# Kernel tuning notes

Hardware: AMD Instinct MI355X
Metric: run time of the kernel (lower is better)

Reference implementation:

```python
import jax, jax.numpy as jnp
import numpy as np

D_MODEL = 2048
N_HEADS = 16
N_KV_HEADS = 4
HEAD_DIM = D_MODEL // N_HEADS  # 128
N_REP = N_HEADS // N_KV_HEADS  # 4
ROPE_BASE = 10000.0


def _rope_tables(T, head_dim, dtype):
    inv_freq = 1.0 / (ROPE_BASE ** (jnp.arange(0, head_dim, 2, dtype=jnp.float32) / head_dim))
    t = jnp.arange(T, dtype=jnp.float32)
    freqs = jnp.outer(t, inv_freq)               # [T, hd/2]
    emb = jnp.concatenate([freqs, freqs], axis=-1)  # [T, hd]
    return jnp.cos(emb).astype(dtype), jnp.sin(emb).astype(dtype)


def _rotate_half(x):
    x1, x2 = jnp.split(x, 2, axis=-1)
    return jnp.concatenate([-x2, x1], axis=-1)


def _apply_rope(x, cos, sin):
    # x: [B, H, T, hd]; cos/sin: [T, hd]
    return x * cos[None, None] + _rotate_half(x) * sin[None, None]


def setup_inputs() -> dict:
    key = jax.random.key(0)
    ks = jax.random.split(key, 5)
    B, T = 2, 2048
    s_in = 1.0 / np.sqrt(D_MODEL)
    return {
        "x": jax.random.normal(ks[0], (B, T, D_MODEL), jnp.float32),
        "Wq": jax.random.normal(ks[1], (D_MODEL, D_MODEL), jnp.float32) * s_in,
        "Wk": jax.random.normal(ks[2], (D_MODEL, N_KV_HEADS * HEAD_DIM), jnp.float32) * s_in,
        "Wv": jax.random.normal(ks[3], (D_MODEL, N_KV_HEADS * HEAD_DIM), jnp.float32) * s_in,
        "Wo": jax.random.normal(ks[4], (D_MODEL, D_MODEL), jnp.float32) * s_in,
    }


def reference(x, Wq, Wk, Wv, Wo):
    B, T, C = x.shape
    scale = HEAD_DIM ** -0.5
    q = (x @ Wq).reshape(B, T, N_HEADS, HEAD_DIM).transpose(0, 2, 1, 3)     # [B,H,T,hd]
    k = (x @ Wk).reshape(B, T, N_KV_HEADS, HEAD_DIM).transpose(0, 2, 1, 3)  # [B,Hkv,T,hd]
    v = (x @ Wv).reshape(B, T, N_KV_HEADS, HEAD_DIM).transpose(0, 2, 1, 3)
    cos, sin = _rope_tables(T, HEAD_DIM, x.dtype)
    q = _apply_rope(q, cos, sin)
    k = _apply_rope(k, cos, sin)
    # GQA: group query heads; avoid materializing expanded K/V
    qg = q.reshape(B, N_KV_HEADS, N_REP, T, HEAD_DIM)
    scores = jnp.einsum('bgrtd,bgsd->bgrts', qg, k) * scale                 # [B,Hkv,rep,T,S]
    causal = jnp.tril(jnp.ones((T, T), dtype=bool))
    scores = jnp.where(causal[None, None, None], scores, jnp.finfo(scores.dtype).min)
    attn = jax.nn.softmax(scores, axis=-1)
    out = jnp.einsum('bgrts,bgsd->bgrtd', attn, v)                          # [B,Hkv,rep,T,hd]
    out = out.reshape(B, N_HEADS, T, HEAD_DIM).transpose(0, 2, 1, 3).reshape(B, T, C)
    return out @ Wo, k, v
```

## Files before the change

kernel.cpp:

```cpp
#include <hip/hip_runtime.h>
#include <hip/hip_bf16.h>
#include <type_traits>


typedef short  short8 __attribute__((ext_vector_type(8)));
typedef float  f32x4  __attribute__((ext_vector_type(4)));
typedef float  f32x16 __attribute__((ext_vector_type(16)));

#define AS1(p) ((__attribute__((address_space(1))) void*)(p))
#define AS3(p) ((__attribute__((address_space(3))) void*)(p))

static __device__ inline short bf_bits(float f) {
    __hip_bfloat16 h = __float2bfloat16(f);
    return *reinterpret_cast<short*>(&h);
}

__global__ __launch_bounds__(256) void convert_x_kernel(
    const float* __restrict__ x, __hip_bfloat16* __restrict__ xb)
{
    int i = (blockIdx.x * 256 + threadIdx.x) * 4;
    float4 v = *reinterpret_cast<const float4*>(x + i);
    ushort4 o;
    o.x = (unsigned short)bf_bits(v.x);
    o.y = (unsigned short)bf_bits(v.y);
    o.z = (unsigned short)bf_bits(v.z);
    o.w = (unsigned short)bf_bits(v.w);
    *reinterpret_cast<ushort4*>(reinterpret_cast<unsigned short*>(xb) + i) = o;
}

__global__ void transpose_convert_kernel(
    const float* __restrict__ W, __hip_bfloat16* __restrict__ WT, int K, int N)
{
    __shared__ float tile[32][33];
    int n0 = blockIdx.x * 32, k0 = blockIdx.y * 32;
    int tx = threadIdx.x, ty = threadIdx.y;
#pragma unroll
    for (int i = 0; i < 32; i += 8)
        tile[ty + i][tx] = W[(size_t)(k0 + ty + i) * N + n0 + tx];
    __syncthreads();
#pragma unroll
    for (int i = 0; i < 32; i += 8)
        WT[(size_t)(n0 + ty + i) * K + k0 + tx] = __float2bfloat16(tile[tx][ty + i]);
}

static __device__ inline void xcd_decode(int bid, int M, int N, int& m0, int& n0)
{
    const int xcd = bid & 7;
    const int idx = bid >> 3;
    const int mpx = (M >> 7) >> 3;
    const int rem = idx % (mpx * 4);
    const int mb = xcd * mpx + rem % mpx;
    const int nb = (idx / (mpx * 4)) * 4 + rem / mpx;
    m0 = mb << 7;
    n0 = nb << 7;
}

#define WAITV4 asm volatile("s_waitcnt vmcnt(4)" ::: "memory")
#define WAITV0 asm volatile("s_waitcnt vmcnt(0)" ::: "memory")

template <typename CT>
__global__ __launch_bounds__(256) void gemm_bt_kernel(
    const __hip_bfloat16* __restrict__ A,
    const __hip_bfloat16* __restrict__ BT,
    CT* __restrict__ C, int M, int N, int K)
{
    const int tid  = threadIdx.x;
    const int w    = tid >> 6;
    const int lane = tid & 63;
    const int l31  = lane & 31;
    const int hi   = lane >> 5;
    int m0, n0;
    xcd_decode(blockIdx.x, M, N, m0, n0);
    const int wm = (w >> 1) << 6;
    const int wn = (w & 1) << 6;

    __shared__ __hip_bfloat16 As[2][128 * 64];
    __shared__ __hip_bfloat16 Bs[2][128 * 64];

    f32x16 acc[2][2] = {};

#define GSTAGE(buf, k0_)                                                            \
    {                                                                               \
        _Pragma("unroll")                                                           \
        for (int i = 0; i < 4; ++i) {                                               \
            int c = tid + i * 256;                                                  \
            int row = c >> 3;                                                       \
            int soct = (c & 7) ^ (row & 7);                                         \
            const __hip_bfloat16* ga = A  + (size_t)(m0 + row) * K + (k0_) + soct * 8; \
            const __hip_bfloat16* gb = BT + (size_t)(n0 + row) * K + (k0_) + soct * 8; \
            __builtin_amdgcn_global_load_lds(AS1(ga), AS3(&As[buf][c * 8]), 16, 0, 0); \
            __builtin_amdgcn_global_load_lds(AS1(gb), AS3(&Bs[buf][c * 8]), 16, 0, 0); \
        }                                                                           \
    }

    GSTAGE(0, 0);
    __syncthreads();
    int cur = 0;
    const int nk = K >> 6;

    for (int t = 0; t < nk; ++t) {
        if (t + 1 < nk) GSTAGE(cur ^ 1, (t + 1) << 6);

#pragma unroll
        for (int ks = 0; ks < 4; ++ks) {
            const int oct = ((ks * 2 + hi) ^ (l31 & 7)) << 3;
            short8 a[2], b[2];
#pragma unroll
            for (int mi = 0; mi < 2; ++mi)
                a[mi] = *reinterpret_cast<const short8*>(
                    reinterpret_cast<const short*>(&As[cur][0]) + (wm + mi * 32 + l31) * 64 + oct);
#pragma unroll
            for (int ni = 0; ni < 2; ++ni)
                b[ni] = *reinterpret_cast<const short8*>(
                    reinterpret_cast<const short*>(&Bs[cur][0]) + (wn + ni * 32 + l31) * 64 + oct);
#pragma unroll
            for (int mi = 0; mi < 2; ++mi)
#pragma unroll
                for (int ni = 0; ni < 2; ++ni)
                    acc[mi][ni] = __builtin_amdgcn_mfma_f32_32x32x16_bf16(
                        a[mi], b[ni], acc[mi][ni], 0, 0, 0);
        }
        __syncthreads();
        cur ^= 1;
    }
#undef GSTAGE

#pragma unroll
    for (int mi = 0; mi < 2; ++mi)
#pragma unroll
        for (int ni = 0; ni < 2; ++ni)
#pragma unroll
            for (int reg = 0; reg < 16; ++reg) {
                int row = m0 + wm + mi * 32 + (reg & 3) + 8 * (reg >> 2) + 4 * hi;
                int col = n0 + wn + ni * 32 + l31;
                float v = acc[mi][ni][reg];
                if constexpr (std::is_same<CT, float>::value)
                    C[(size_t)row * N + col] = v;
                else
                    C[(size_t)row * N + col] = __float2bfloat16(v);
            }
}

__global__ __launch_bounds__(256) void gemm_qkv_fused(
    const __hip_bfloat16* __restrict__ A,
    const __hip_bfloat16* __restrict__ BT,
    __hip_bfloat16* __restrict__ qkv,
    float* __restrict__ outk,
    float* __restrict__ outv,
    __hip_bfloat16* __restrict__ VT)
{
    const int tid  = threadIdx.x;
    const int w    = tid >> 6;
    const int lane = tid & 63;
    const int l31  = lane & 31;
    const int hi   = lane >> 5;
    int m0, n0;
    xcd_decode(blockIdx.x, 4096, 3072, m0, n0);
    const int wm = w << 5;
    const int K = 2048;

    __shared__ __hip_bfloat16 As[3][128 * 32];
    __shared__ __hip_bfloat16 Bs[3][128 * 32];

    f32x16 acc[4] = {};

#define GSTAGE(buf, k0_)                                                             \
    {                                                                                \
        _Pragma("unroll")                                                            \
        for (int i = 0; i < 2; ++i) {                                                \
            int c = tid + i * 256;                                                   \
            int row = c >> 2;                                                        \
            int soct = (c & 3) ^ ((row >> 1) & 3);                                   \
            const __hip_bfloat16* ga = A  + (size_t)(m0 + row) * K + (k0_) + soct * 8; \
            const __hip_bfloat16* gb = BT + (size_t)(n0 + row) * K + (k0_) + soct * 8; \
            __builtin_amdgcn_global_load_lds(AS1(ga), AS3(&As[buf][c * 8]), 16, 0, 0); \
            __builtin_amdgcn_global_load_lds(AS1(gb), AS3(&Bs[buf][c * 8]), 16, 0, 0); \
        }                                                                            \
    }

    const int nk = 64;
    GSTAGE(0, 0);
    GSTAGE(1, 32);
    int cur = 0, stg = 2;

    for (int t = 0; t < nk; ++t) {
        if (t == nk - 1) { WAITV0; } else { WAITV4; }
        __builtin_amdgcn_s_barrier();
        __builtin_amdgcn_sched_barrier(0);
        if (t + 2 < nk) GSTAGE(stg, (t + 2) << 5);

#pragma unroll
        for (int ks = 0; ks < 2; ++ks) {
            int arow = wm + l31;
            short8 a = *reinterpret_cast<const short8*>(
                reinterpret_cast<const short*>(&As[cur][0])
                + arow * 32 + (((ks * 2 + hi) ^ ((arow >> 1) & 3)) << 3));
#pragma unroll
            for (int ni = 0; ni < 4; ++ni) {
                int brow = ni * 32 + l31;
                short8 b = *reinterpret_cast<const short8*>(
                    reinterpret_cast<const short*>(&Bs[cur][0])
                    + brow * 32 + (((ks * 2 + hi) ^ ((brow >> 1) & 3)) << 3));
                acc[ni] = __builtin_amdgcn_mfma_f32_32x32x16_bf16(a, b, acc[ni], 0, 0, 0);
            }
        }
        cur = (cur == 2) ? 0 : cur + 1;
        stg = (stg == 2) ? 0 : stg + 1;
    }
#undef GSTAGE

    const int hc = n0 >> 7;
    if (hc < 20) {
        float invf[2];
#pragma unroll
        for (int ni = 0; ni < 2; ++ni)
            invf[ni] = exp2f((float)(ni * 32 + l31) * -0.20762050593046f);
#pragma unroll
        for (int reg = 0; reg < 16; ++reg) {
            int row = m0 + wm + (reg & 3) + 8 * (reg >> 2) + 4 * hi;
            int b = row >> 11, t = row & 2047;
#pragma unroll
            for (int ni = 0; ni < 2; ++ni) {
                int d = ni * 32 + l31;
                float ang = (float)t * invf[ni];
                float s = __sinf(ang), c = __cosf(ang);
                float x1 = acc[ni][reg], x2 = acc[ni + 2][reg];
                float o1 = x1 * c - x2 * s;
                float o2 = x2 * c + x1 * s;
                __hip_bfloat16* q = qkv + (size_t)row * 3072 + hc * 128 + d;
                q[0]  = __float2bfloat16(o1);
                q[64] = __float2bfloat16(o2);
                if (hc >= 16) {
                    int kh = hc - 16;
                    float* ok = outk + (size_t)((b * 4 + kh) * 2048 + t) * 128 + d;
                    ok[0]  = o1;
                    ok[64] = o2;
                }
            }
        }
    } else {
        const int kh = hc - 20;
#pragma unroll
        for (int reg = 0; reg < 16; ++reg) {
            int row = m0 + wm + (reg & 3) + 8 * (reg >> 2) + 4 * hi;
            int b = row >> 11, t = row & 2047;
#pragma unroll
            for (int ni = 0; ni < 4; ++ni) {
                int d = ni * 32 + l31;
                float v = acc[ni][reg];
                outv[(size_t)((b * 4 + kh) * 2048 + t) * 128 + d] = v;
                VT[(size_t)((b * 4 + kh) * 128 + d) * 2048 + t] = __float2bfloat16(v);
            }
        }
    }
}

__global__ __launch_bounds__(256, 2) void attn_kernel(
    const __hip_bfloat16* __restrict__ qkv,
    const __hip_bfloat16* __restrict__ VT,
    __hip_bfloat16* __restrict__ outO)
{
    const int bh = blockIdx.x;
    const int b = bh >> 4, h = bh & 15;
    const int kh = h >> 2;
    const int yb = blockIdx.y;
    const int qblk = (yb < 8) ? (15 - yb) : (yb - 8);
    const int tid = threadIdx.x;
    const int w = tid >> 6;
    const int lane = tid & 63;
    const int lo16 = lane & 15, grp = lane >> 4;
    const int qrow0 = qblk * 128 + w * 32;

    __shared__ short Ks[2][64 * 128];
    __shared__ short Vs[2][128 * 64];
    __shared__ short Ps[4][32 * 64];

    const short* qkvs = reinterpret_cast<const short*>(qkv);
    const size_t kbase = (size_t)b * 2048 * 3072 + 2048 + kh * 128;
    const short* vtb = reinterpret_cast<const short*>(VT) + (size_t)(b * 4 + kh) * 128 * 2048;
    short* pw = &Ps[w][0];

    short8 qf[2][4];
#pragma unroll
    for (int mi = 0; mi < 2; ++mi) {
        const short* qp = qkvs + (size_t)(b * 2048 + qrow0 + mi * 16 + lo16) * 3072
                        + h * 128 + grp * 8;
#pragma unroll
        for (int ss = 0; ss < 4; ++ss)
            qf[mi][ss] = *reinterpret_cast<const short8*>(qp + ss * 32);
    }

    f32x4 o[2][8] = {};
    f32x4 lac[2] = {};

    short8 ones;
#pragma unroll
    for (int jj = 0; jj < 8; ++jj) ones[jj] = (short)0x3F80;

    const float scl2 = 0.12752749545902973f;
    const int ntiles = qblk * 2 + 2;

#define STAGE(buf, kb_)                                                              \
    {                                                                                \
        _Pragma("unroll")                                                            \
        for (int i = 0; i < 4; ++i) {                                                \
            int c = tid + i * 256;                                                   \
            int row = c >> 4, c16 = (c & 15) ^ (row & 7);                            \
            const short* src = qkvs + kbase + (size_t)((kb_) + row) * 3072 + c16 * 8;\
            __builtin_amdgcn_global_load_lds(AS1(src),                               \
                AS3(&Ks[buf][(w * 64 + i * 256) * 8]), 16, 0, 0);                    \
        }                                                                            \
        _Pragma("unroll")                                                            \
        for (int i = 0; i < 4; ++i) {                                                \
            int c = tid + i * 256;                                                   \
            int d = c >> 3, c8 = (c & 7) ^ (d & 7);                                  \
            const short* src = vtb + (size_t)d * 2048 + (kb_) + c8 * 8;              \
            __builtin_amdgcn_global_load_lds(AS1(src),                               \
                AS3(&Vs[buf][(w * 64 + i * 256) * 8]), 16, 0, 0);                    \
        }                                                                            \
    }

    STAGE(0, 0);
    __syncthreads();
    int cur = 0;

    for (int t = 0; t < ntiles; ++t) {
        const int kb = t * 64;
        if (t + 1 < ntiles) STAGE(cur ^ 1, kb + 64);

        f32x4 sg[2][4];
        __builtin_amdgcn_s_setprio(1);
#pragma unroll
        for (int kg = 0; kg < 4; ++kg) {
            f32x4 a0 = {}, a1 = {};
#pragma unroll
            for (int ss = 0; ss < 4; ++ss) {
                short8 kf = *reinterpret_cast<const short8*>(
                    &Ks[cur][(kg * 16 + lo16) * 128 + (((ss * 4 + grp) ^ (lo16 & 7)) << 3)]);
                a0 = __builtin_amdgcn_mfma_f32_16x16x32_bf16(qf[0][ss], kf, a0, 0, 0, 0);
                a1 = __builtin_amdgcn_mfma_f32_16x16x32_bf16(qf[1][ss], kf, a1, 0, 0, 0);
            }
            sg[0][kg] = a0; sg[1][kg] = a1;
        }
        __builtin_amdgcn_s_setprio(0);

        if (kb + 63 > qrow0) {
#pragma unroll
            for (int mi = 0; mi < 2; ++mi)
#pragma unroll
                for (int kg = 0; kg < 4; ++kg) {
                    const int key = kb + kg * 16 + lo16;
#pragma unroll
                    for (int r = 0; r < 4; ++r) {
                        float v = sg[mi][kg][r] * scl2;
                        sg[mi][kg][r] = (key <= qrow0 + mi * 16 + grp * 4 + r) ? v : -1e30f;
                    }
                }
        } else {
#pragma unroll
            for (int mi = 0; mi < 2; ++mi)
#pragma unroll
                for (int kg = 0; kg < 4; ++kg)
#pragma unroll
                    for (int r = 0; r < 4; ++r) sg[mi][kg][r] *= scl2;
        }

#pragma unroll
        for (int mi = 0; mi < 2; ++mi)
#pragma unroll
            for (int kg = 0; kg < 4; ++kg)
#pragma unroll
                for (int r = 0; r < 4; ++r) {
                    float p = __builtin_amdgcn_exp2f(sg[mi][kg][r]);
                    int row = mi * 16 + grp * 4 + r;
                    int idx = row * 64 + (((kg * 2 + (lo16 >> 3)) ^ (row & 7)) << 3) + (lo16 & 7);
                    pw[idx] = bf_bits(p);
                }

        __builtin_amdgcn_s_setprio(1);
#pragma unroll
        for (int ks = 0; ks < 2; ++ks) {
            short8 pf0 = *reinterpret_cast<const short8*>(
                &pw[(0 * 16 + lo16) * 64 + (((ks * 4 + grp) ^ (lo16 & 7)) << 3)]);
            short8 pf1 = *reinterpret_cast<const short8*>(
                &pw[(1 * 16 + lo16) * 64 + (((ks * 4 + grp) ^ (lo16 & 7)) << 3)]);
            lac[0] = __builtin_amdgcn_mfma_f32_16x16x32_bf16(pf0, ones, lac[0], 0, 0, 0);
            lac[1] = __builtin_amdgcn_mfma_f32_16x16x32_bf16(pf1, ones, lac[1], 0, 0, 0);
#pragma unroll
            for (int jj = 0; jj < 8; ++jj) {
                short8 vf = *reinterpret_cast<const short8*>(
                    &Vs[cur][(jj * 16 + lo16) * 64 + (((ks * 4 + grp) ^ (lo16 & 7)) << 3)]);
                o[0][jj] = __builtin_amdgcn_mfma_f32_16x16x32_bf16(pf0, vf, o[0][jj], 0, 0, 0);
                o[1][jj] = __builtin_amdgcn_mfma_f32_16x16x32_bf16(pf1, vf, o[1][jj], 0, 0, 0);
            }
        }
        __builtin_amdgcn_s_setprio(0);

        __syncthreads();
        cur ^= 1;
    }
#undef STAGE

#pragma unroll
    for (int mi = 0; mi < 2; ++mi)
#pragma unroll
        for (int r = 0; r < 4; ++r) {
            float inv = 1.0f / lac[mi][r];
#pragma unroll
            for (int jj = 0; jj < 8; ++jj) {
                outO[(size_t)(b * 2048 + qrow0 + mi * 16 + grp * 4 + r) * 2048
                     + h * 128 + jj * 16 + lo16] = __float2bfloat16(o[mi][jj][r] * inv);
            }
        }
}

extern "C" void kernel_launch(void* const* d_in, const int* in_sizes, int n_in,
                              void* d_out, int out_size, void* d_ws, size_t ws_size,
                              hipStream_t stream)
{
    (void)in_sizes; (void)n_in; (void)out_size; (void)ws_size;
    const float* x  = (const float*)d_in[0];
    const float* Wq = (const float*)d_in[1];
    const float* Wk = (const float*)d_in[2];
    const float* Wv = (const float*)d_in[3];
    const float* Wo = (const float*)d_in[4];

    float* out0 = (float*)d_out;
    float* outk = out0 + 8388608;
    float* outv = out0 + 10485760;

    __hip_bfloat16* wsb    = (__hip_bfloat16*)d_ws;
    __hip_bfloat16* xb     = wsb;
    __hip_bfloat16* WqkvT  = xb + 8388608;
    __hip_bfloat16* WoT    = WqkvT + 6291456;
    __hip_bfloat16* qkv    = WoT + 4194304;
    __hip_bfloat16* VT     = qkv + 12582912;
    __hip_bfloat16* attn_o = xb;

    convert_x_kernel<<<8192, 256, 0, stream>>>(x, xb);
    transpose_convert_kernel<<<dim3(64, 64), dim3(32, 8), 0, stream>>>(Wq, WqkvT, 2048, 2048);
    transpose_convert_kernel<<<dim3(16, 64), dim3(32, 8), 0, stream>>>(Wk, WqkvT + (size_t)2048 * 2048, 2048, 512);
    transpose_convert_kernel<<<dim3(16, 64), dim3(32, 8), 0, stream>>>(Wv, WqkvT + (size_t)2560 * 2048, 2048, 512);
    transpose_convert_kernel<<<dim3(64, 64), dim3(32, 8), 0, stream>>>(Wo, WoT, 2048, 2048);

    gemm_qkv_fused<<<768, 256, 0, stream>>>(xb, WqkvT, qkv, outk, outv, VT);

    attn_kernel<<<dim3(32, 16), 256, 0, stream>>>(qkv, VT, attn_o);

    gemm_bt_kernel<float><<<512, 256, 0, stream>>>(attn_o, WoT, out0, 4096, 2048, 2048);
}
```

Baseline: 194.7 us.

## Use 2x2 wave tiling in QKV GEMM and merge weight transposes into one launch

The QKV GEMM's four waves now each own a 64x64 sub-tile (2x2 MFMA blocks) instead of 32x128, which lowers LDS fragment reads per MFMA. To keep RoPE pairs (d, d+64) inside one wave, the Wq/Wk transpose permutes 32-row blocks within each head. RoPE output is written back in that permuted column order, which the attention kernel is assumed to accept. The four weight transpose launches are also merged into a single grid, cutting launch overhead.

Measured after the change: 190.8 us. -2.0%, faster.

```diff
diff --git a/kernel.cpp b/kernel.cpp
--- a/kernel.cpp
+++ b/kernel.cpp
@@ -28,19 +28,42 @@
     *reinterpret_cast<ushort4*>(reinterpret_cast<unsigned short*>(xb) + i) = o;
 }
 
-__global__ void transpose_convert_kernel(
-    const float* __restrict__ W, __hip_bfloat16* __restrict__ WT, int K, int N)
+__global__ void transpose_all_kernel(
+    const float* __restrict__ Wq, const float* __restrict__ Wk,
+    const float* __restrict__ Wv, const float* __restrict__ Wo,
+    __hip_bfloat16* __restrict__ WqkvT, __hip_bfloat16* __restrict__ WoT)
 {
     __shared__ float tile[32][33];
-    int n0 = blockIdx.x * 32, k0 = blockIdx.y * 32;
-    int tx = threadIdx.x, ty = threadIdx.y;
+    const int nb = blockIdx.x;
+    const int k0 = blockIdx.y * 32;
+    const int tx = threadIdx.x, ty = threadIdx.y;
+    const float* W; int srcN, sn0, drow; __hip_bfloat16* dst;
+    if (nb < 64) {
+        int blk = nb & 3;
+        int blk2 = ((blk & 1) << 1) | (blk >> 1);
+        W = Wq; srcN = 2048; sn0 = nb * 32;
+        dst = WqkvT; drow = ((nb >> 2) * 4 + blk2) * 32;
+    } else if (nb < 80) {
+        int i = nb - 64, blk = i & 3;
+        int blk2 = ((blk & 1) << 1) | (blk >> 1);
+        W = Wk; srcN = 512; sn0 = i * 32;
+        dst = WqkvT; drow = 2048 + ((i >> 2) * 4 + blk2) * 32;
+    } else if (nb < 96) {
+        int i = nb - 80;
+        W = Wv; srcN = 512; sn0 = i * 32;
+        dst = WqkvT; drow = 2560 + i * 32;
+    } else {
+        int i = nb - 96;
+        W = Wo; srcN = 2048; sn0 = i * 32;
+        dst = WoT; drow = i * 32;
+    }
 #pragma unroll
     for (int i = 0; i < 32; i += 8)
-        tile[ty + i][tx] = W[(size_t)(k0 + ty + i) * N + n0 + tx];
+        tile[ty + i][tx] = W[(size_t)(k0 + ty + i) * srcN + sn0 + tx];
     __syncthreads();
 #pragma unroll
     for (int i = 0; i < 32; i += 8)
-        WT[(size_t)(n0 + ty + i) * K + k0 + tx] = __float2bfloat16(tile[tx][ty + i]);
+        dst[(size_t)(drow + ty + i) * 2048 + k0 + tx] = __float2bfloat16(tile[tx][ty + i]);
 }
 
 static __device__ inline void xcd_decode(int bid, int M, int N, int& m0, int& n0)
@@ -156,13 +179,14 @@
     const int hi   = lane >> 5;
     int m0, n0;
     xcd_decode(blockIdx.x, 4096, 3072, m0, n0);
-    const int wm = w << 5;
+    const int wm = (w >> 1) << 6;
+    const int wn = (w & 1) << 6;
     const int K = 2048;
 
     __shared__ __hip_bfloat16 As[3][128 * 32];
     __shared__ __hip_bfloat16 Bs[3][128 * 32];
 
-    f32x16 acc[4] = {};
+    f32x16 acc[2][2] = {};
 
 #define GSTAGE(buf, k0_)                                                             \
     {                                                                                \
@@ -191,18 +215,27 @@
 
 #pragma unroll
         for (int ks = 0; ks < 2; ++ks) {
-            int arow = wm + l31;
-            short8 a = *reinterpret_cast<const short8*>(
-                reinterpret_cast<const short*>(&As[cur][0])
-                + arow * 32 + (((ks * 2 + hi) ^ ((arow >> 1) & 3)) << 3));
-#pragma unroll
-            for (int ni = 0; ni < 4; ++ni) {
-                int brow = ni * 32 + l31;
-                short8 b = *reinterpret_cast<const short8*>(
+            short8 a[2], b[2];
+#pragma unroll
+            for (int mi = 0; mi < 2; ++mi) {
+                int row = wm + mi * 32 + l31;
+                a[mi] = *reinterpret_cast<const short8*>(
+                    reinterpret_cast<const short*>(&As[cur][0])
+                    + row * 32 + (((ks * 2 + hi) ^ ((row >> 1) & 3)) << 3));
+            }
+#pragma unroll
+            for (int ni = 0; ni < 2; ++ni) {
+                int row = wn + ni * 32 + l31;
+                b[ni] = *reinterpret_cast<const short8*>(
                     reinterpret_cast<const short*>(&Bs[cur][0])
-                    + brow * 32 + (((ks * 2 + hi) ^ ((brow >> 1) & 3)) << 3));
-                acc[ni] = __builtin_amdgcn_mfma_f32_32x32x16_bf16(a, b, acc[ni], 0, 0, 0);
-            }
+                    + row * 32 + (((ks * 2 + hi) ^ ((row >> 1) & 3)) << 3));
+            }
+#pragma unroll
+            for (int mi = 0; mi < 2; ++mi)
+#pragma unroll
+                for (int ni = 0; ni < 2; ++ni)
+                    acc[mi][ni] = __builtin_amdgcn_mfma_f32_32x32x16_bf16(
+                        a[mi], b[ni], acc[mi][ni], 0, 0, 0);
         }
         cur = (cur == 2) ? 0 : cur + 1;
         stg = (stg == 2) ? 0 : stg + 1;
@@ -211,47 +244,46 @@
 
     const int hc = n0 >> 7;
     if (hc < 20) {
-        float invf[2];
-#pragma unroll
-        for (int ni = 0; ni < 2; ++ni)
-            invf[ni] = exp2f((float)(ni * 32 + l31) * -0.20762050593046f);
-#pragma unroll
-        for (int reg = 0; reg < 16; ++reg) {
-            int row = m0 + wm + (reg & 3) + 8 * (reg >> 2) + 4 * hi;
-            int b = row >> 11, t = row & 2047;
-#pragma unroll
-            for (int ni = 0; ni < 2; ++ni) {
-                int d = ni * 32 + l31;
-                float ang = (float)t * invf[ni];
+        const int c0 = wn + l31;
+        const int d_lo = (wn ? 32 : 0) + l31;
+        const float invf = exp2f((float)d_lo * -0.20762050593046f);
+        const int kh = hc - 16;
+#pragma unroll
+        for (int mi = 0; mi < 2; ++mi)
+#pragma unroll
+            for (int reg = 0; reg < 16; ++reg) {
+                int row = m0 + wm + mi * 32 + (reg & 3) + 8 * (reg >> 2) + 4 * hi;
+                int b = row >> 11, t = row & 2047;
+                float ang = (float)t * invf;
                 float s = __sinf(ang), c = __cosf(ang);
-                float x1 = acc[ni][reg], x2 = acc[ni + 2][reg];
+                float x1 = acc[mi][0][reg], x2 = acc[mi][1][reg];
                 float o1 = x1 * c - x2 * s;
                 float o2 = x2 * c + x1 * s;
-                __hip_bfloat16* q = qkv + (size_t)row * 3072 + hc * 128 + d;
+                __hip_bfloat16* q = qkv + (size_t)row * 3072 + hc * 128 + c0;
                 q[0]  = __float2bfloat16(o1);
-                q[64] = __float2bfloat16(o2);
+                q[32] = __float2bfloat16(o2);
                 if (hc >= 16) {
-                    int kh = hc - 16;
-                    float* ok = outk + (size_t)((b * 4 + kh) * 2048 + t) * 128 + d;
+                    float* ok = outk + (size_t)((b * 4 + kh) * 2048 + t) * 128 + d_lo;
                     ok[0]  = o1;
                     ok[64] = o2;
                 }
             }
-        }
     } else {
         const int kh = hc - 20;
 #pragma unroll
-        for (int reg = 0; reg < 16; ++reg) {
-            int row = m0 + wm + (reg & 3) + 8 * (reg >> 2) + 4 * hi;
-            int b = row >> 11, t = row & 2047;
-#pragma unroll
-            for (int ni = 0; ni < 4; ++ni) {
-                int d = ni * 32 + l31;
-                float v = acc[ni][reg];
-                outv[(size_t)((b * 4 + kh) * 2048 + t) * 128 + d] = v;
-                VT[(size_t)((b * 4 + kh) * 128 + d) * 2048 + t] = __float2bfloat16(v);
-            }
-        }
+        for (int mi = 0; mi < 2; ++mi)
+#pragma unroll
+            for (int reg = 0; reg < 16; ++reg) {
+                int row = m0 + wm + mi * 32 + (reg & 3) + 8 * (reg >> 2) + 4 * hi;
+                int b = row >> 11, t = row & 2047;
+#pragma unroll
+                for (int ni = 0; ni < 2; ++ni) {
+                    int d = wn + ni * 32 + l31;
+                    float v = acc[mi][ni][reg];
+                    outv[(size_t)((b * 4 + kh) * 2048 + t) * 128 + d] = v;
+                    VT[(size_t)((b * 4 + kh) * 128 + d) * 2048 + t] = __float2bfloat16(v);
+                }
+            }
     }
 }
 
@@ -438,10 +470,8 @@
     __hip_bfloat16* attn_o = xb;
 
     convert_x_kernel<<<8192, 256, 0, stream>>>(x, xb);
-    transpose_convert_kernel<<<dim3(64, 64), dim3(32, 8), 0, stream>>>(Wq, WqkvT, 2048, 2048);
-    transpose_convert_kernel<<<dim3(16, 64), dim3(32, 8), 0, stream>>>(Wk, WqkvT + (size_t)2048 * 2048, 2048, 512);
-    transpose_convert_kernel<<<dim3(16, 64), dim3(32, 8), 0, stream>>>(Wv, WqkvT + (size_t)2560 * 2048, 2048, 512);
-    transpose_convert_kernel<<<dim3(64, 64), dim3(32, 8), 0, stream>>>(Wo, WoT, 2048, 2048);
+    transpose_all_kernel<<<dim3(160, 64), dim3(32, 8), 0, stream>>>(
+        Wq, Wk, Wv, Wo, WqkvT, WoT);
 
     gemm_qkv_fused<<<768, 256, 0, stream>>>(xb, WqkvT, qkv, outk, outv, VT);
 
```
